# Kernel optimization log

Hardware: AMD Instinct MI355X
Metric: run time of the kernel (lower is better)

## Reference

```python
import jax, jax.numpy as jnp
import numpy as np

B, S, DM = 2, 1024, 2048          # batch, seq_len, hidden_size
H, HKV, D = 16, 8, 128            # heads, kv heads, head_dim
G = H // HKV                      # kv groups
W = 256                           # bmojo window_size
EPS = 1e-6
SCALE = D ** -0.5                 # softmax_scale (set because qk_norm is used)
NEG = -1e30


def _rmsnorm(x, g):
    # per-head RMSNorm over last dim D
    return x * jax.lax.rsqrt(jnp.mean(x * x, axis=-1, keepdims=True) + EPS) * g


def _rope(x, cos, sin):
    # x: [B,S,H,D]; cos/sin: [B,S,D]
    c = cos[:, :, None, :]
    s = sin[:, :, None, :]
    d2 = x.shape[-1] // 2
    x1, x2 = x[..., :d2], x[..., d2:]
    rot = jnp.concatenate([-x2, x1], axis=-1)
    return x * c + rot * s


def setup_inputs() -> dict:
    key = jax.random.key(0)
    ks = jax.random.split(key, 24)
    std = DM ** -0.5

    def lin_w(k, out_d, in_d):
        return jax.random.normal(k, (out_d, in_d), jnp.float32) * std

    def lin_b(k, out_d):
        return jax.random.normal(k, (out_d,), jnp.float32) * 0.01

    inp = {"hidden_states": jax.random.normal(ks[0], (B, S, DM), jnp.float32)}

    # standard RoPE cos/sin tables (theta=10000), shape [B,S,D]
    pos = jnp.arange(S, dtype=jnp.float32)[:, None]
    inv = 1.0 / (10000.0 ** (jnp.arange(0, D, 2, dtype=jnp.float32) / D))
    emb = jnp.concatenate([pos * inv[None, :]] * 2, axis=-1)  # [S,D]
    inp["cos"] = jnp.broadcast_to(jnp.cos(emb)[None], (B, S, D))
    inp["sin"] = jnp.broadcast_to(jnp.sin(emb)[None], (B, S, D))

    # tied (in-context) projections; attention_bias default -> qkv bias True, o bias False
    inp["Wq"] = lin_w(ks[1], H * D, DM);    inp["bq"] = lin_b(ks[2], H * D)
    inp["Wk"] = lin_w(ks[3], HKV * D, DM);  inp["bk"] = lin_b(ks[4], HKV * D)
    inp["Wv"] = lin_w(ks[5], HKV * D, DM);  inp["bv"] = lin_b(ks[6], HKV * D)
    # untied (fading) projections (tie_attn_weights=False)
    inp["Wq2"] = lin_w(ks[7], H * D, DM);   inp["bq2"] = lin_b(ks[8], H * D)
    inp["Wk2"] = lin_w(ks[9], HKV * D, DM); inp["bk2"] = lin_b(ks[10], HKV * D)
    inp["Wv2"] = lin_w(ks[11], HKV * D, DM); inp["bv2"] = lin_b(ks[12], HKV * D)
    inp["Wo"] = lin_w(ks[13], DM, H * D)
    # QK RMSNorm gammas (near-one so grads are nontrivial)
    inp["gq"] = 1.0 + 0.02 * jax.random.normal(ks[14], (D,), jnp.float32)
    inp["gk"] = 1.0 + 0.02 * jax.random.normal(ks[15], (D,), jnp.float32)
    inp["gq2"] = 1.0 + 0.02 * jax.random.normal(ks[16], (D,), jnp.float32)
    inp["gk2"] = 1.0 + 0.02 * jax.random.normal(ks[17], (D,), jnp.float32)
    return inp


def _qkv(x, cos, sin, Wq, bq, Wk, bk, Wv, bv, gq, gk):
    b, s, _ = x.shape
    q = (x @ Wq.T + bq).reshape(b, s, H, D)
    k = (x @ Wk.T + bk).reshape(b, s, HKV, D)
    v = (x @ Wv.T + bv).reshape(b, s, HKV, D)
    q = _rmsnorm(q, gq)
    k = _rmsnorm(k, gk)
    q = _rope(q, cos, sin)
    k = _rope(k, cos, sin)
    # GQA: expand kv heads to H
    k = jnp.repeat(k, G, axis=2)
    v = jnp.repeat(v, G, axis=2)
    return q, k, v


def reference(hidden_states, cos, sin, Wq, bq, Wk, bk, Wv, bv,
              Wq2, bq2, Wk2, bk2, Wv2, bv2, Wo, gq, gk, gq2, gk2):
    # in-context (tied) and fading (untied) projection paths
    q_ic, k_ic, v_ic = _qkv(hidden_states, cos, sin, Wq, bq, Wk, bk, Wv, bv, gq, gk)
    q_f, k_f, v_f = _qkv(hidden_states, cos, sin, Wq2, bq2, Wk2, bk2, Wv2, bv2, gq2, gk2)

    s_ic = jnp.einsum('bqhd,bkhd->bhqk', q_ic, k_ic) * SCALE
    s_f = jnp.einsum('bqhd,bkhd->bhqk', q_f, k_f) * SCALE

    i = jnp.arange(S)[:, None]
    j = jnp.arange(S)[None, :]
    dij = i - j
    in_window = (dij >= 0) & (dij < W)   # sliding window (window_size-1 lookback + self)
    fading = dij >= W                    # older tokens handled by fading memory

    s_ic = jnp.where(in_window, s_ic, NEG)
    s_f = jnp.where(fading, s_f, NEG)

    # joint softmax over the union of window and fading key sets
    p = jax.nn.softmax(jnp.concatenate([s_ic, s_f], axis=-1), axis=-1)  # [B,H,S,2S]
    p_ic, p_f = p[..., :S], p[..., S:]

    out = jnp.einsum('bhqk,bkhd->bqhd', p_ic, v_ic) \
        + jnp.einsum('bhqk,bkhd->bqhd', p_f, v_f)
    out = out.reshape(B, S, H * D)
    return out @ Wo.T
```

## Files before the change

### kernel.cpp

```cpp
#include <hip/hip_runtime.h>
#include <cstdint>
#include <cstddef>

#define B_    2
#define S_    1024
#define DM_   2048
#define H_    16
#define HKV_  8
#define D_    128
#define W_    256
#define NPROJ 8192
#define MROWS 2048
#define SCALE_ 0.08838834764831845f
#define MNEG  -3.0e38f
#define FIXM  16.0f

typedef float  f32x4  __attribute__((ext_vector_type(4)));
typedef __bf16 bf16x8 __attribute__((ext_vector_type(8)));
typedef __bf16 bf16x4 __attribute__((ext_vector_type(4)));

__device__ __forceinline__ void gload16(const void* g, void* l) {
  __builtin_amdgcn_global_load_lds((const __attribute__((address_space(1))) unsigned int*)g,
                                   (__attribute__((address_space(3))) unsigned int*)l, 16, 0, 0);
}

__global__ __launch_bounds__(256) void cvt_all(
    const float* __restrict__ x,  const float* __restrict__ wq,  const float* __restrict__ wk,
    const float* __restrict__ wv, const float* __restrict__ wq2, const float* __restrict__ wk2,
    const float* __restrict__ wv2,const float* __restrict__ wo,
    const float* __restrict__ bq, const float* __restrict__ bk, const float* __restrict__ bv,
    const float* __restrict__ bq2,const float* __restrict__ bk2,const float* __restrict__ bv2,
    __bf16* __restrict__ xb, __bf16* __restrict__ wall, __bf16* __restrict__ wob,
    float* __restrict__ biasA) {
  const int i = blockIdx.x * 256 + threadIdx.x;
  if (i >= 6293504) return;
  if (i >= 6291456) {
    const int j = i - 6291456, flat = j * 4;
    const int set = flat >> 12, off = flat & 4095;
    const float* bsrc; int boff;
    if (off < 2048)      { bsrc = set ? bq2 : bq; boff = off; }
    else if (off < 3072) { bsrc = set ? bk2 : bk; boff = off - 2048; }
    else                 { bsrc = set ? bv2 : bv; boff = off - 3072; }
    ((f32x4*)biasA)[j] = *(const f32x4*)&bsrc[boff];
    return;
  }
  const float* s; __bf16* d;
  if      (i < 1048576) { s = x   + (size_t)i * 4;              d = xb   + (size_t)i * 4; }
  else if (i < 2097152) { s = wq  + (size_t)(i - 1048576) * 4;  d = wall + (size_t)(i - 1048576) * 4; }
  else if (i < 2621440) { s = wk  + (size_t)(i - 2097152) * 4;  d = wall + 4194304  + (size_t)(i - 2097152) * 4; }
  else if (i < 3145728) { s = wv  + (size_t)(i - 2621440) * 4;  d = wall + 6291456  + (size_t)(i - 2621440) * 4; }
  else if (i < 4194304) { s = wq2 + (size_t)(i - 3145728) * 4;  d = wall + 8388608  + (size_t)(i - 3145728) * 4; }
  else if (i < 4718592) { s = wk2 + (size_t)(i - 4194304) * 4;  d = wall + 12582912 + (size_t)(i - 4194304) * 4; }
  else if (i < 5242880) { s = wv2 + (size_t)(i - 4718592) * 4;  d = wall + 14680064 + (size_t)(i - 4718592) * 4; }
  else                  { s = wo  + (size_t)(i - 5242880) * 4;  d = wob  + (size_t)(i - 5242880) * 4; }
  float4 f = *(const float4*)s;
  bf16x4 o;
  o.x = (__bf16)f.x; o.y = (__bf16)f.y; o.z = (__bf16)f.z; o.w = (__bf16)f.w;
  *(bf16x4*)d = o;
}

__global__ __launch_bounds__(512) void gemm_qkv(const __bf16* __restrict__ A,
                                                const __bf16* __restrict__ Bm,
                                                __bf16* __restrict__ Cv,
                                                const float* __restrict__ bias,
                                                int N, int K, int nxp) {
  __shared__ __align__(16) char lds[131072];
  const int tid = threadIdx.x, lane = tid & 63, wid = tid >> 6;
  const int bid = blockIdx.x, xcd = bid & 7, ii = bid >> 3;
  const int x = xcd * nxp + (ii % nxp);
  const int y = ii / nxp;
  const int m0 = y * 256, n0 = x * 256;
  const int wm = (wid >> 2) * 128, wn = (wid & 3) * 64;
  const int g = lane >> 4, c16 = lane & 15;

  int sRow[8], sCol[8]; bool sA[8];
#pragma unroll
  for (int p = 0; p < 8; ++p) {
    const int o = p * 8192 + tid * 16, ro = o & 32767;
    sA[p]   = o < 32768;
    sRow[p] = ro >> 7;
    sCol[p] = (((ro & 127) ^ ((sRow[p] & 7) << 4))) >> 1;
  }

  auto stage2 = [&](int k0, int buf, int q) {
#pragma unroll
    for (int pp = 0; pp < 2; ++pp) {
      const int p = q * 2 + pp;
      const __bf16* src = sA[p] ? &A [(size_t)(m0 + sRow[p]) * K + k0 + sCol[p]]
                                : &Bm[(size_t)(n0 + sRow[p]) * K + k0 + sCol[p]];
      gload16(src, lds + buf * 65536 + p * 8192 + wid * 1024);
    }
  };
  auto rdA = [&](int buf, int mi, int kk) -> bf16x8 {
    const int r = wm + mi * 16 + c16;
    return *(const bf16x8*)(lds + buf * 65536 + r * 128 + ((kk * 64 + g * 16) ^ ((r & 7) << 4)));
  };
  auto rdB = [&](int buf, int ni, int kk) -> bf16x8 {
    const int r = wn + ni * 16 + c16;
    return *(const bf16x8*)(lds + buf * 65536 + 32768 + r * 128 + ((kk * 64 + g * 16) ^ ((r & 7) << 4)));
  };

  f32x4 acc[8][4] = {};
  const int NT = K >> 6;

#pragma unroll
  for (int q = 0; q < 4; ++q) stage2(0, 0, q);
  asm volatile("s_waitcnt vmcnt(0)" ::: "memory");
  __builtin_amdgcn_s_barrier();

  for (int t = 0; t < NT; ++t) {
    const int buf = t & 1, k0 = t * 64;
    bf16x8 b[4][2];
#pragma unroll
    for (int q = 0; q < 4; ++q) {
      bf16x8 a[2][2];
#pragma unroll
      for (int dm = 0; dm < 2; ++dm)
#pragma unroll
        for (int kk = 0; kk < 2; ++kk) a[dm][kk] = rdA(buf, q * 2 + dm, kk);
      if (q == 0) {
#pragma unroll
        for (int ni = 0; ni < 4; ++ni)
#pragma unroll
          for (int kk = 0; kk < 2; ++kk) b[ni][kk] = rdB(buf, ni, kk);
      }
      if (t + 1 < NT) stage2(k0 + 64, buf ^ 1, q);
      __builtin_amdgcn_s_barrier();
      __builtin_amdgcn_s_setprio(1);
#pragma unroll
      for (int dm = 0; dm < 2; ++dm)
#pragma unroll
        for (int ni = 0; ni < 4; ++ni)
#pragma unroll
          for (int kk = 0; kk < 2; ++kk)
            acc[q * 2 + dm][ni] =
              __builtin_amdgcn_mfma_f32_16x16x32_bf16(a[dm][kk], b[ni][kk], acc[q * 2 + dm][ni], 0, 0, 0);
      __builtin_amdgcn_s_setprio(0);
    }
    if (t + 1 < NT) { asm volatile("s_waitcnt vmcnt(0)" ::: "memory"); }
    __builtin_amdgcn_s_barrier();
  }

#pragma unroll
  for (int mi = 0; mi < 8; ++mi)
#pragma unroll
    for (int ni = 0; ni < 4; ++ni) {
      const int gn = n0 + wn + ni * 16 + c16;
      const float bv = bias[gn];
#pragma unroll
      for (int r = 0; r < 4; ++r) {
        const int gm = m0 + wm + mi * 16 + g * 4 + r;
        Cv[(size_t)gm * N + gn] = (__bf16)(acc[mi][ni][r] + bv);
      }
    }
}

__global__ __launch_bounds__(256) void gemm_out(const __bf16* __restrict__ A,
                                                const __bf16* __restrict__ Bm,
                                                float* __restrict__ Cv) {
  __shared__ __align__(16) char lds[65536];
  const int tid = threadIdx.x, lane = tid & 63, wid = tid >> 6;
  const int bid = blockIdx.x, xcd = bid & 7, ii = bid >> 3;
  const int x = xcd * 2 + (ii & 1);
  const int y = ii >> 1;
  const int m0 = y * 128, n0 = x * 128;
  const int wm = (wid >> 1) * 64, wn = (wid & 1) * 64;
  const int g = lane >> 4, c16 = lane & 15;
  const int K = DM_, N = DM_;

  const int tR = tid >> 3;
  const int tC = (((tid & 7) * 16) ^ ((tR & 7) << 4)) >> 1;

  auto stageP = [&](int k0, int buf, int p) {
    const __bf16* src = (p < 4) ? &A [(size_t)(m0 + p * 32 + tR) * K + k0 + tC]
                                : &Bm[(size_t)(n0 + (p - 4) * 32 + tR) * K + k0 + tC];
    gload16(src, lds + buf * 32768 + p * 4096 + wid * 1024);
  };
  auto rdA = [&](int buf, int mi, int kk) -> bf16x8 {
    const int r = wm + mi * 16 + c16;
    return *(const bf16x8*)(lds + buf * 32768 + r * 128 + ((kk * 64 + g * 16) ^ ((r & 7) << 4)));
  };
  auto rdB = [&](int buf, int ni, int kk) -> bf16x8 {
    const int r = wn + ni * 16 + c16;
    return *(const bf16x8*)(lds + buf * 32768 + 16384 + r * 128 + ((kk * 64 + g * 16) ^ ((r & 7) << 4)));
  };

  f32x4 acc[4][4] = {};
  const int NT = K >> 6;

#pragma unroll
  for (int p = 0; p < 8; ++p) stageP(0, 0, p);
  asm volatile("s_waitcnt vmcnt(0)" ::: "memory");
  __builtin_amdgcn_s_barrier();

  for (int t = 0; t < NT; ++t) {
    const int buf = t & 1, k0 = t * 64;
    bf16x8 b[4][2];
#pragma unroll
    for (int q = 0; q < 4; ++q) {
      bf16x8 a[2];
#pragma unroll
      for (int kk = 0; kk < 2; ++kk) a[kk] = rdA(buf, q, kk);
      if (q == 0) {
#pragma unroll
        for (int ni = 0; ni < 4; ++ni)
#pragma unroll
          for (int kk = 0; kk < 2; ++kk) b[ni][kk] = rdB(buf, ni, kk);
      }
      if (t + 1 < NT) { stageP(k0 + 64, buf ^ 1, q * 2); stageP(k0 + 64, buf ^ 1, q * 2 + 1); }
      __builtin_amdgcn_s_barrier();
      __builtin_amdgcn_s_setprio(1);
#pragma unroll
      for (int ni = 0; ni < 4; ++ni)
#pragma unroll
        for (int kk = 0; kk < 2; ++kk)
          acc[q][ni] = __builtin_amdgcn_mfma_f32_16x16x32_bf16(a[kk], b[ni][kk], acc[q][ni], 0, 0, 0);
      __builtin_amdgcn_s_setprio(0);
    }
    if (t + 1 < NT) { asm volatile("s_waitcnt vmcnt(0)" ::: "memory"); }
    __builtin_amdgcn_s_barrier();
  }

#pragma unroll
  for (int mi = 0; mi < 4; ++mi)
#pragma unroll
    for (int ni = 0; ni < 4; ++ni) {
      const int gn = n0 + wn + ni * 16 + c16;
#pragma unroll
      for (int r = 0; r < 4; ++r) {
        const int gm = m0 + wm + mi * 16 + g * 4 + r;
        Cv[(size_t)gm * N + gn] = acc[mi][ni][r];
      }
    }
}

__global__ __launch_bounds__(256) void post_all(const __bf16* __restrict__ proj,
    const float* __restrict__ cosg, const float* __restrict__ sing,
    const float* __restrict__ gq, const float* __restrict__ gk,
    const float* __restrict__ gq2, const float* __restrict__ gk2,
    __bf16* __restrict__ Q0, __bf16* __restrict__ K0,
    __bf16* __restrict__ Q1, __bf16* __restrict__ K1,
    __bf16* __restrict__ Vt0, __bf16* __restrict__ Vt1) {
  __shared__ __bf16 T[64][136];
  const int tid = threadIdx.x;
  if (blockIdx.x < 2048) {
    const int row  = blockIdx.x;
    const int b    = row >> 10;
    const int s    = row & 1023;
    const int lane = tid & 63, wid = tid >> 6;
    const float* cp = cosg + (size_t)row * D_;
    const float* sp = sing + (size_t)row * D_;
    const float c1 = cp[lane], c2 = cp[lane + 64];
    const float s1 = sp[lane], s2 = sp[lane + 64];

    for (int hi = wid; hi < 48; hi += 4) {
      const int  set  = hi >= 24 ? 1 : 0;
      const int  loc  = hi - set * 24;
      const bool isq  = loc < 16;
      const int  head = isq ? loc : loc - 16;
      const __bf16* src = proj + (size_t)row * NPROJ + set * 4096 + (isq ? head * 128 : 2048 + head * 128);
      const float* gv   = set ? (isq ? gq2 : gk2) : (isq ? gq : gk);
      __bf16* dst       = set ? (isq ? Q1 : K1) : (isq ? Q0 : K0);
      const int nheads  = isq ? H_ : HKV_;
      const size_t didx = (((size_t)b * nheads + head) * S_ + s) * D_;
      float x1 = (float)src[lane], x2 = (float)src[lane + 64];
      float ss = x1 * x1 + x2 * x2;
#pragma unroll
      for (int o = 1; o < 64; o <<= 1) ss += __shfl_xor(ss, o);
      const float rr = rsqrtf(ss * (1.f / 128.f) + 1e-6f);
      const float n1 = x1 * rr * gv[lane];
      const float n2 = x2 * rr * gv[lane + 64];
      dst[didx + lane]      = (__bf16)(n1 * c1 - n2 * s1);
      dst[didx + lane + 64] = (__bf16)(n2 * c2 + n1 * s2);
    }
  } else {
    const int bid = blockIdx.x - 2048;
    const int st = bid & 15;
    const int hk = (bid >> 4) & 7;
    const int b  = (bid >> 7) & 1;
    const int sg = bid >> 8;
    const int s0 = st * 64;
    const size_t prow = ((size_t)(b * S_ + s0)) * NPROJ + sg * 4096 + 3072 + hk * 128;
    const int r = tid >> 4, c = (tid & 15) * 8;
#pragma unroll
    for (int pass = 0; pass < 4; ++pass) {
      const int rr = pass * 16 + r;
      *(bf16x8*)&T[rr][c] = *(const bf16x8*)&proj[prow + (size_t)rr * NPROJ + c];
    }
    __syncthreads();
    __bf16* Vt = (sg ? Vt1 : Vt0) + (size_t)(b * HKV_ + hk) * D_ * S_;
    const int d = tid >> 1, half = tid & 1;
#pragma unroll
    for (int q8 = 0; q8 < 4; ++q8) {
      const int sb = half * 32 + q8 * 8;
      bf16x8 v;
#pragma unroll
      for (int k = 0; k < 8; ++k) v[k] = T[sb + k][d];
      *(bf16x8*)&Vt[(size_t)d * S_ + s0 + sb] = v;
    }
  }
}

__global__ __launch_bounds__(256) void attn_fused(
    const __bf16* __restrict__ Q0, const __bf16* __restrict__ K0g, const __bf16* __restrict__ Vt0,
    const __bf16* __restrict__ Q1, const __bf16* __restrict__ K1g, const __bf16* __restrict__ Vt1,
    __bf16* __restrict__ AO) {
  __shared__ __bf16 KsL[2][2][32 * 128];
  __shared__ __bf16 VtL[2][2][128 * 32];
  __shared__ __bf16 Ps[4][16][40];

  const int tid = threadIdx.x, lane = tid & 63, wid = tid >> 6;
  const int bid = blockIdx.x;
  const int xcd = bid & 7, jj = bid >> 3;
  const int combo = xcd * 2 + (jj >> 4);
  const int b = combo >> 3, hk = combo & 7;
  const int h = hk * 2 + ((jj >> 3) & 1);
  const int pq = jj & 7;
  const int qtA = pq, qtB = 15 - pq;
  const int ntA = 2 * qtA + 2;
  const int ntT = 34;

  const int g = lane >> 4, kc = lane & 15;
  const size_t qoff  = (size_t)(b * H_ + h) * S_ * D_;
  const size_t koff  = (size_t)(b * HKV_ + hk) * S_ * D_;
  const size_t vtoff = (size_t)(b * HKV_ + hk) * D_ * S_;

  int kRow[2], kCol[2], vD[2], vJ[2];
#pragma unroll
  for (int p = 0; p < 2; ++p) {
    const int boff = (wid * 2 + p) * 1024 + lane * 16;
    kRow[p] = boff >> 8;
    kCol[p] = ((boff & 255) ^ ((kRow[p] & 7) << 4)) >> 1;
    vD[p]   = boff >> 6;
    vJ[p]   = (boff & 63) >> 1;
  }

  bf16x8 qf0[4], qf1[4];
  auto loadQ = [&](int qw) {
    const int qrow = qw + kc;
#pragma unroll
    for (int c = 0; c < 4; ++c) {
      qf0[c] = *(const bf16x8*)&Q0[qoff + (size_t)qrow * D_ + c * 32 + g * 8];
      qf1[c] = *(const bf16x8*)&Q1[qoff + (size_t)qrow * D_ + c * 32 + g * 8];
    }
  };

  float rs[4];
  f32x4 o[8];
  auto resetS = [&]() {
#pragma unroll
    for (int r = 0; r < 4; ++r) rs[r] = 0.f;
#pragma unroll
    for (int ch = 0; ch < 8; ++ch)
#pragma unroll
      for (int r = 0; r < 4; ++r) o[ch][r] = 0.f;
  };

  auto stage = [&](int qb2, int t, int bufi) {
    const int j0 = t * 32;
    const bool nic = (j0 >= qb2 - 286);
    const bool nf  = (j0 <= qb2 - 193);
#pragma unroll
    for (int p = 0; p < 2; ++p) {
      const int ko = wid * 2048 + p * 1024;
      if (nic) {
        gload16(K0g + koff + (size_t)(j0 + kRow[p]) * D_ + kCol[p], (char*)&KsL[bufi][0][0] + ko);
        gload16(Vt0 + vtoff + (size_t)vD[p] * S_ + j0 + vJ[p],      (char*)&VtL[bufi][0][0] + ko);
      }
      if (nf) {
        gload16(K1g + koff + (size_t)(j0 + kRow[p]) * D_ + kCol[p], (char*)&KsL[bufi][1][0] + ko);
        gload16(Vt1 + vtoff + (size_t)vD[p] * S_ + j0 + vJ[p],      (char*)&VtL[bufi][1][0] + ko);
      }
    }
  };

  auto qk = [&](const __bf16* Kb, const bf16x8 qf[4], f32x4 sv[2]) {
#pragma unroll
    for (int c = 0; c < 4; ++c) {
      const int r0 = kc, r1 = kc + 16;
      const bf16x8 k0f = *(const bf16x8*)((const char*)Kb + r0 * 256 + ((c * 64 + g * 16) ^ ((r0 & 7) << 4)));
      const bf16x8 k1f = *(const bf16x8*)((const char*)Kb + r1 * 256 + ((c * 64 + g * 16) ^ ((r1 & 7) << 4)));
      sv[0] = __builtin_amdgcn_mfma_f32_16x16x32_bf16(qf[c], k0f, sv[0], 0, 0, 0);
      sv[1] = __builtin_amdgcn_mfma_f32_16x16x32_bf16(qf[c], k1f, sv[1], 0, 0, 0);
    }
  };

  auto dopv = [&](const f32x4 sv[2], const __bf16* Vtb) {
#pragma unroll
    for (int nh = 0; nh < 2; ++nh) {
      const int col = kc + nh * 16, c8 = col >> 3, cw = col & 7;
#pragma unroll
      for (int r = 0; r < 4; ++r)
        Ps[wid][g * 4 + r][((c8 ^ g) << 3) + cw] = (__bf16)sv[nh][r];
    }
    asm volatile("s_waitcnt lgkmcnt(0)" ::: "memory");
    const bf16x8 pa = *(const bf16x8*)&Ps[wid][kc][(g ^ (kc >> 2)) << 3];
#pragma unroll
    for (int ch = 0; ch < 8; ++ch) {
      const bf16x8 vb = *(const bf16x8*)&Vtb[(ch * 16 + kc) * 32 + g * 8];
      o[ch] = __builtin_amdgcn_mfma_f32_16x16x32_bf16(pa, vb, o[ch], 0, 0, 0);
    }
  };

  auto writeOut = [&](int qw2) {
    float ell[4];
#pragma unroll
    for (int r = 0; r < 4; ++r) ell[r] = rs[r];
#pragma unroll
    for (int ofs = 1; ofs < 16; ofs <<= 1)
#pragma unroll
      for (int r = 0; r < 4; ++r) ell[r] += __shfl_xor(ell[r], ofs);
#pragma unroll
    for (int r = 0; r < 4; ++r) {
      const float inv = 1.f / ell[r];
      const size_t orow = ((size_t)b * S_ + qw2 + g * 4 + r) * (size_t)(H_ * D_) + h * D_;
#pragma unroll
      for (int ch = 0; ch < 8; ++ch)
        AO[orow + ch * 16 + kc] = (__bf16)(o[ch][r] * inv);
    }
  };

  int qb = qtA * 64, qw = qb + wid * 16;
  loadQ(qw);
  resetS();
  stage(qb, 0, 0);
  asm volatile("s_waitcnt vmcnt(0)" ::: "memory");
  __builtin_amdgcn_s_barrier();
  int cur = 0;

  for (int it = 0; it < ntT; ++it) {
    const int t = (it >= ntA) ? it - ntA : it;
    if (it + 1 < ntT) {
      const bool hN = (it + 1 >= ntA);
      stage(hN ? qtB * 64 : qtA * 64, hN ? it + 1 - ntA : it + 1, cur ^ 1);
    }
    const int j0 = t * 32;
    if (j0 <= qw + 15) {
      const bool w_ic = (j0 >= qw - 286);
      const bool w_f  = (j0 <= qw - 241);

      f32x4 sic[2] = {}, sfd[2] = {};
      if (w_ic) {
        qk(&KsL[cur][0][0], qf0, sic);
#pragma unroll
        for (int nh = 0; nh < 2; ++nh)
#pragma unroll
          for (int r = 0; r < 4; ++r) {
            const int dij = (qw + g * 4 + r) - (j0 + kc + nh * 16);
            const float arg = (dij >= 0 && dij < W_) ? fmaf(sic[nh][r], SCALE_, -FIXM) : MNEG;
            const float p = __expf(arg);
            rs[r] += p; sic[nh][r] = p;
          }
        dopv(sic, &VtL[cur][0][0]);
      }
      if (w_f) {
        qk(&KsL[cur][1][0], qf1, sfd);
#pragma unroll
        for (int nh = 0; nh < 2; ++nh)
#pragma unroll
          for (int r = 0; r < 4; ++r) {
            const int dij = (qw + g * 4 + r) - (j0 + kc + nh * 16);
            const float arg = (dij >= W_) ? fmaf(sfd[nh][r], SCALE_, -FIXM) : MNEG;
            const float p = __expf(arg);
            rs[r] += p; sfd[nh][r] = p;
          }
        dopv(sfd, &VtL[cur][1][0]);
      }
    }
    asm volatile("s_waitcnt vmcnt(0)" ::: "memory");
    __builtin_amdgcn_s_barrier();
    cur ^= 1;

    if (it + 1 == ntA) {
      writeOut(qw);
      resetS();
      qb = qtB * 64; qw = qb + wid * 16;
      loadQ(qw);
    }
  }
  writeOut(qw);
}

extern "C" void kernel_launch(void* const* d_in, const int* in_sizes, int n_in,
                              void* d_out, int out_size, void* d_ws, size_t ws_size,
                              hipStream_t stream) {
  (void)in_sizes; (void)n_in; (void)out_size; (void)ws_size;
  const float* hidden = (const float*)d_in[0];
  const float* cosg   = (const float*)d_in[1];
  const float* sing   = (const float*)d_in[2];
  const float* Wq  = (const float*)d_in[3];
  const float* bq  = (const float*)d_in[4];
  const float* Wk  = (const float*)d_in[5];
  const float* bk  = (const float*)d_in[6];
  const float* Wv  = (const float*)d_in[7];
  const float* bv  = (const float*)d_in[8];
  const float* Wq2 = (const float*)d_in[9];
  const float* bq2 = (const float*)d_in[10];
  const float* Wk2 = (const float*)d_in[11];
  const float* bk2 = (const float*)d_in[12];
  const float* Wv2 = (const float*)d_in[13];
  const float* bv2 = (const float*)d_in[14];
  const float* Wo  = (const float*)d_in[15];
  const float* gq  = (const float*)d_in[16];
  const float* gk  = (const float*)d_in[17];
  const float* gq2 = (const float*)d_in[18];
  const float* gk2 = (const float*)d_in[19];

  char* w = (char*)d_ws;
  __bf16* Xb    = (__bf16*)(w);
  __bf16* Wall  = (__bf16*)(w + 8388608);
  __bf16* Wob   = (__bf16*)(w + 41943040);
  float*  biasA = (float*) (w + 50331648);
  __bf16* proj  = (__bf16*)(w + 50364416);
  __bf16* AO  = Xb;
  __bf16* Q0  = Wall;
  __bf16* Q1  = Wall + 4194304;
  __bf16* K0  = Wall + 8388608;
  __bf16* K1  = Wall + 10485760;
  __bf16* Vt0 = Wall + 12582912;
  __bf16* Vt1 = Wall + 14680064;

  cvt_all<<<24584, 256, 0, stream>>>(hidden, Wq, Wk, Wv, Wq2, Wk2, Wv2, Wo,
                                     bq, bk, bv, bq2, bk2, bv2,
                                     Xb, Wall, Wob, biasA);
  gemm_qkv<<<256, 512, 0, stream>>>(Xb, Wall, proj, biasA, NPROJ, DM_, 4);
  post_all<<<2560, 256, 0, stream>>>(proj, cosg, sing, gq, gk, gq2, gk2,
                                     Q0, K0, Q1, K1, Vt0, Vt1);
  attn_fused<<<256, 256, 0, stream>>>(Q0, K0, Vt0, Q1, K1, Vt1, AO);
  gemm_out<<<256, 256, 0, stream>>>(AO, Wob, (float*)d_out);
}
```

Measured before the change: 177.5 us.

## Restructure GEMM mainloops into 4-stage, 32-wide K pipeline with two-ahead prefetch

Both the QKV projection GEMM and the output GEMM move from a double-buffered 64-wide K step to four LDS stages of 32-wide K slices, prefetching two steps ahead. Each wait now allows some loads to stay in flight (vmcnt(4)) instead of draining all of them. The LDS swizzle changes to a rotation-based layout suited to 64-byte rows. The goal is to hide global-load latency better and avoid full drains every iteration. In exchange there are twice as many barriers per unit of K, and the waitcnt bookkeeping is more fragile.

```diff
diff --git a/kernel.cpp b/kernel.cpp
--- a/kernel.cpp
+++ b/kernel.cpp
@@ -73,72 +73,79 @@
   const int wm = (wid >> 2) * 128, wn = (wid & 3) * 64;
   const int g = lane >> 4, c16 = lane & 15;
 
-  int sRow[8], sCol[8]; bool sA[8];
-#pragma unroll
-  for (int p = 0; p < 8; ++p) {
-    const int o = p * 8192 + tid * 16, ro = o & 32767;
-    sA[p]   = o < 32768;
-    sRow[p] = ro >> 7;
-    sCol[p] = (((ro & 127) ^ ((sRow[p] & 7) << 4))) >> 1;
-  }
-
-  auto stage2 = [&](int k0, int buf, int q) {
-#pragma unroll
-    for (int pp = 0; pp < 2; ++pp) {
-      const int p = q * 2 + pp;
-      const __bf16* src = sA[p] ? &A [(size_t)(m0 + sRow[p]) * K + k0 + sCol[p]]
-                                : &Bm[(size_t)(n0 + sRow[p]) * K + k0 + sCol[p]];
-      gload16(src, lds + buf * 65536 + p * 8192 + wid * 1024);
-    }
-  };
-  auto rdA = [&](int buf, int mi, int kk) -> bf16x8 {
+  int sRow[4], sColE[4]; bool sA4[4];
+#pragma unroll
+  for (int st = 0; st < 4; ++st) {
+    const int o = st * 8192 + tid * 16;
+    sA4[st]  = o < 16384;
+    sRow[st] = (o & 16383) >> 6;
+    const int q = (o >> 4) & 3;
+    sColE[st] = ((q - (sRow[st] >> 1)) & 3) << 3;
+  }
+
+  auto stageStep = [&](int j, int st) {
+    const int s = j & 3;
+    const __bf16* src = sA4[st] ? &A [(size_t)(m0 + sRow[st]) * K + j * 32 + sColE[st]]
+                                : &Bm[(size_t)(n0 + sRow[st]) * K + j * 32 + sColE[st]];
+    gload16(src, lds + s * 32768 + st * 8192 + wid * 1024);
+  };
+  auto rdA = [&](int s, int mi) -> bf16x8 {
     const int r = wm + mi * 16 + c16;
-    return *(const bf16x8*)(lds + buf * 65536 + r * 128 + ((kk * 64 + g * 16) ^ ((r & 7) << 4)));
-  };
-  auto rdB = [&](int buf, int ni, int kk) -> bf16x8 {
+    const int q = (g + (r >> 1)) & 3;
+    return *(const bf16x8*)(lds + s * 32768 + r * 64 + q * 16);
+  };
+  auto rdB = [&](int s, int ni) -> bf16x8 {
     const int r = wn + ni * 16 + c16;
-    return *(const bf16x8*)(lds + buf * 65536 + 32768 + r * 128 + ((kk * 64 + g * 16) ^ ((r & 7) << 4)));
+    const int q = (g + (r >> 1)) & 3;
+    return *(const bf16x8*)(lds + s * 32768 + 16384 + r * 64 + q * 16);
   };
 
   f32x4 acc[8][4] = {};
-  const int NT = K >> 6;
-
-#pragma unroll
-  for (int q = 0; q < 4; ++q) stage2(0, 0, q);
-  asm volatile("s_waitcnt vmcnt(0)" ::: "memory");
+  const int NS = K >> 5;
+
+#pragma unroll
+  for (int st = 0; st < 4; ++st) stageStep(0, st);
+#pragma unroll
+  for (int st = 0; st < 4; ++st) stageStep(1, st);
+  asm volatile("s_waitcnt vmcnt(4)" ::: "memory");
   __builtin_amdgcn_s_barrier();
 
-  for (int t = 0; t < NT; ++t) {
-    const int buf = t & 1, k0 = t * 64;
-    bf16x8 b[4][2];
-#pragma unroll
-    for (int q = 0; q < 4; ++q) {
-      bf16x8 a[2][2];
-#pragma unroll
-      for (int dm = 0; dm < 2; ++dm)
-#pragma unroll
-        for (int kk = 0; kk < 2; ++kk) a[dm][kk] = rdA(buf, q * 2 + dm, kk);
-      if (q == 0) {
-#pragma unroll
-        for (int ni = 0; ni < 4; ++ni)
-#pragma unroll
-          for (int kk = 0; kk < 2; ++kk) b[ni][kk] = rdB(buf, ni, kk);
-      }
-      if (t + 1 < NT) stage2(k0 + 64, buf ^ 1, q);
+  for (int j = 0; j < NS; ++j) {
+    const int s = j & 3;
+    const bool more = (j + 2 < NS);
+    bf16x8 bfr[4], a[4];
+
+#pragma unroll
+    for (int mi = 0; mi < 4; ++mi) a[mi] = rdA(s, mi);
+#pragma unroll
+    for (int ni = 0; ni < 4; ++ni) bfr[ni] = rdB(s, ni);
+    if (more) { stageStep(j + 2, 0); stageStep(j + 2, 1); }
+    __builtin_amdgcn_s_barrier();
+    __builtin_amdgcn_s_setprio(1);
+#pragma unroll
+    for (int mi = 0; mi < 4; ++mi)
+#pragma unroll
+      for (int ni = 0; ni < 4; ++ni)
+        acc[mi][ni] = __builtin_amdgcn_mfma_f32_16x16x32_bf16(a[mi], bfr[ni], acc[mi][ni], 0, 0, 0);
+    __builtin_amdgcn_s_setprio(0);
+
+#pragma unroll
+    for (int mi = 0; mi < 4; ++mi) a[mi] = rdA(s, 4 + mi);
+    if (more) { stageStep(j + 2, 2); stageStep(j + 2, 3); }
+    __builtin_amdgcn_s_barrier();
+    __builtin_amdgcn_s_setprio(1);
+#pragma unroll
+    for (int mi = 0; mi < 4; ++mi)
+#pragma unroll
+      for (int ni = 0; ni < 4; ++ni)
+        acc[4 + mi][ni] = __builtin_amdgcn_mfma_f32_16x16x32_bf16(a[mi], bfr[ni], acc[4 + mi][ni], 0, 0, 0);
+    __builtin_amdgcn_s_setprio(0);
+
+    if (j + 1 < NS) {
+      if (more) { asm volatile("s_waitcnt vmcnt(4)" ::: "memory"); }
+      else      { asm volatile("s_waitcnt vmcnt(0)" ::: "memory"); }
       __builtin_amdgcn_s_barrier();
-      __builtin_amdgcn_s_setprio(1);
-#pragma unroll
-      for (int dm = 0; dm < 2; ++dm)
-#pragma unroll
-        for (int ni = 0; ni < 4; ++ni)
-#pragma unroll
-          for (int kk = 0; kk < 2; ++kk)
-            acc[q * 2 + dm][ni] =
-              __builtin_amdgcn_mfma_f32_16x16x32_bf16(a[dm][kk], b[ni][kk], acc[q * 2 + dm][ni], 0, 0, 0);
-      __builtin_amdgcn_s_setprio(0);
-    }
-    if (t + 1 < NT) { asm volatile("s_waitcnt vmcnt(0)" ::: "memory"); }
-    __builtin_amdgcn_s_barrier();
+    }
   }
 
 #pragma unroll
@@ -168,57 +175,79 @@
   const int g = lane >> 4, c16 = lane & 15;
   const int K = DM_, N = DM_;
 
-  const int tR = tid >> 3;
-  const int tC = (((tid & 7) * 16) ^ ((tR & 7) << 4)) >> 1;
-
-  auto stageP = [&](int k0, int buf, int p) {
-    const __bf16* src = (p < 4) ? &A [(size_t)(m0 + p * 32 + tR) * K + k0 + tC]
-                                : &Bm[(size_t)(n0 + (p - 4) * 32 + tR) * K + k0 + tC];
-    gload16(src, lds + buf * 32768 + p * 4096 + wid * 1024);
-  };
-  auto rdA = [&](int buf, int mi, int kk) -> bf16x8 {
+  int sRow[4], sColE[4]; bool sA4[4];
+#pragma unroll
+  for (int st = 0; st < 4; ++st) {
+    const int o = st * 4096 + tid * 16;
+    sA4[st]  = o < 8192;
+    sRow[st] = (o & 8191) >> 6;
+    const int q = (o >> 4) & 3;
+    sColE[st] = ((q - (sRow[st] >> 1)) & 3) << 3;
+  }
+
+  auto stageStep = [&](int j, int st) {
+    const int s = j & 3;
+    const __bf16* src = sA4[st] ? &A [(size_t)(m0 + sRow[st]) * K + j * 32 + sColE[st]]
+                                : &Bm[(size_t)(n0 + sRow[st]) * K + j * 32 + sColE[st]];
+    gload16(src, lds + s * 16384 + st * 4096 + wid * 1024);
+  };
+  auto rdA = [&](int s, int mi) -> bf16x8 {
     const int r = wm + mi * 16 + c16;
-    return *(const bf16x8*)(lds + buf * 32768 + r * 128 + ((kk * 64 + g * 16) ^ ((r & 7) << 4)));
-  };
-  auto rdB = [&](int buf, int ni, int kk) -> bf16x8 {
+    const int q = (g + (r >> 1)) & 3;
+    return *(const bf16x8*)(lds + s * 16384 + r * 64 + q * 16);
+  };
+  auto rdB = [&](int s, int ni) -> bf16x8 {
     const int r = wn + ni * 16 + c16;
-    return *(const bf16x8*)(lds + buf * 32768 + 16384 + r * 128 + ((kk * 64 + g * 16) ^ ((r & 7) << 4)));
+    const int q = (g + (r >> 1)) & 3;
+    return *(const bf16x8*)(lds + s * 16384 + 8192 + r * 64 + q * 16);
   };
 
   f32x4 acc[4][4] = {};
-  const int NT = K >> 6;
-
-#pragma unroll
-  for (int p = 0; p < 8; ++p) stageP(0, 0, p);
-  asm volatile("s_waitcnt vmcnt(0)" ::: "memory");
+  const int NS = K >> 5;
+
+#pragma unroll
+  for (int st = 0; st < 4; ++st) stageStep(0, st);
+#pragma unroll
+  for (int st = 0; st < 4; ++st) stageStep(1, st);
+  asm volatile("s_waitcnt vmcnt(4)" ::: "memory");
   __builtin_amdgcn_s_barrier();
 
-  for (int t = 0; t < NT; ++t) {
-    const int buf = t & 1, k0 = t * 64;
-    bf16x8 b[4][2];
-#pragma unroll
-    for (int q = 0; q < 4; ++q) {
-      bf16x8 a[2];
-#pragma unroll
-      for (int kk = 0; kk < 2; ++kk) a[kk] = rdA(buf, q, kk);
-      if (q == 0) {
-#pragma unroll
-        for (int ni = 0; ni < 4; ++ni)
-#pragma unroll
-          for (int kk = 0; kk < 2; ++kk) b[ni][kk] = rdB(buf, ni, kk);
-      }
-      if (t + 1 < NT) { stageP(k0 + 64, buf ^ 1, q * 2); stageP(k0 + 64, buf ^ 1, q * 2 + 1); }
+  for (int j = 0; j < NS; ++j) {
+    const int s = j & 3;
+    const bool more = (j + 2 < NS);
+    bf16x8 bfr[4], a[2];
+
+#pragma unroll
+    for (int mi = 0; mi < 2; ++mi) a[mi] = rdA(s, mi);
+#pragma unroll
+    for (int ni = 0; ni < 4; ++ni) bfr[ni] = rdB(s, ni);
+    if (more) { stageStep(j + 2, 0); stageStep(j + 2, 1); }
+    __builtin_amdgcn_s_barrier();
+    __builtin_amdgcn_s_setprio(1);
+#pragma unroll
+    for (int mi = 0; mi < 2; ++mi)
+#pragma unroll
+      for (int ni = 0; ni < 4; ++ni)
+        acc[mi][ni] = __builtin_amdgcn_mfma_f32_16x16x32_bf16(a[mi], bfr[ni], acc[mi][ni], 0, 0, 0);
+    __builtin_amdgcn_s_setprio(0);
+
+#pragma unroll
+    for (int mi = 0; mi < 2; ++mi) a[mi] = rdA(s, 2 + mi);
+    if (more) { stageStep(j + 2, 2); stageStep(j + 2, 3); }
+    __builtin_amdgcn_s_barrier();
+    __builtin_amdgcn_s_setprio(1);
+#pragma unroll
+    for (int mi = 0; mi < 2; ++mi)
+#pragma unroll
+      for (int ni = 0; ni < 4; ++ni)
+        acc[2 + mi][ni] = __builtin_amdgcn_mfma_f32_16x16x32_bf16(a[mi], bfr[ni], acc[2 + mi][ni], 0, 0, 0);
+    __builtin_amdgcn_s_setprio(0);
+
+    if (j + 1 < NS) {
+      if (more) { asm volatile("s_waitcnt vmcnt(4)" ::: "memory"); }
+      else      { asm volatile("s_waitcnt vmcnt(0)" ::: "memory"); }
       __builtin_amdgcn_s_barrier();
-      __builtin_amdgcn_s_setprio(1);
-#pragma unroll
-      for (int ni = 0; ni < 4; ++ni)
-#pragma unroll
-        for (int kk = 0; kk < 2; ++kk)
-          acc[q][ni] = __builtin_amdgcn_mfma_f32_16x16x32_bf16(a[kk], b[ni][kk], acc[q][ni], 0, 0, 0);
-      __builtin_amdgcn_s_setprio(0);
-    }
-    if (t + 1 < NT) { asm volatile("s_waitcnt vmcnt(0)" ::: "memory"); }
-    __builtin_amdgcn_s_barrier();
+    }
   }
 
 #pragma unroll
```

Measured after the change: 179.2 us. No clear change (+1.0%).

## Switch QKV GEMM to triple-buffered 32-wide K stages with new LDS swizzle

Applied to the files above, without the earlier changes.

The QKV projection GEMM drops its double-buffered 64-wide K tiles and uses a three-stage ring of 32-wide K tiles. Loads run two stages ahead and are throttled with partial vmcnt waits, so each step needs one barrier instead of five. The LDS layout moves to 64-byte rows with a rotation-based swizzle to avoid bank conflicts, and LDS use drops from 128KB to 96KB. The cost is twice as many loop iterations with less MFMA work per barrier, and the new swizzle may conflict differently.

```diff
diff --git a/kernel.cpp b/kernel.cpp
--- a/kernel.cpp
+++ b/kernel.cpp
@@ -64,7 +64,7 @@
                                                 __bf16* __restrict__ Cv,
                                                 const float* __restrict__ bias,
                                                 int N, int K, int nxp) {
-  __shared__ __align__(16) char lds[131072];
+  __shared__ __align__(16) char lds[98304];
   const int tid = threadIdx.x, lane = tid & 63, wid = tid >> 6;
   const int bid = blockIdx.x, xcd = bid & 7, ii = bid >> 3;
   const int x = xcd * nxp + (ii % nxp);
@@ -73,72 +73,67 @@
   const int wm = (wid >> 2) * 128, wn = (wid & 3) * 64;
   const int g = lane >> 4, c16 = lane & 15;
 
-  int sRow[8], sCol[8]; bool sA[8];
-#pragma unroll
-  for (int p = 0; p < 8; ++p) {
-    const int o = p * 8192 + tid * 16, ro = o & 32767;
-    sA[p]   = o < 32768;
-    sRow[p] = ro >> 7;
-    sCol[p] = (((ro & 127) ^ ((sRow[p] & 7) << 4))) >> 1;
-  }
-
-  auto stage2 = [&](int k0, int buf, int q) {
-#pragma unroll
-    for (int pp = 0; pp < 2; ++pp) {
-      const int p = q * 2 + pp;
-      const __bf16* src = sA[p] ? &A [(size_t)(m0 + sRow[p]) * K + k0 + sCol[p]]
-                                : &Bm[(size_t)(n0 + sRow[p]) * K + k0 + sCol[p]];
-      gload16(src, lds + buf * 65536 + p * 8192 + wid * 1024);
-    }
-  };
-  auto rdA = [&](int buf, int mi, int kk) -> bf16x8 {
+  int sRow[4], sColE[4]; bool sA4[4];
+#pragma unroll
+  for (int st = 0; st < 4; ++st) {
+    const int o = st * 8192 + tid * 16;
+    sA4[st]  = o < 16384;
+    sRow[st] = (o & 16383) >> 6;
+    const int q = (o >> 4) & 3;
+    sColE[st] = ((q - (sRow[st] >> 1)) & 3) << 3;
+  }
+
+  auto stageTile = [&](int j) {
+    const int s = j % 3;
+#pragma unroll
+    for (int st = 0; st < 4; ++st) {
+      const __bf16* src = sA4[st] ? &A [(size_t)(m0 + sRow[st]) * K + j * 32 + sColE[st]]
+                                  : &Bm[(size_t)(n0 + sRow[st]) * K + j * 32 + sColE[st]];
+      gload16(src, lds + s * 32768 + st * 8192 + wid * 1024);
+    }
+  };
+  auto rdA = [&](int s, int mi) -> bf16x8 {
     const int r = wm + mi * 16 + c16;
-    return *(const bf16x8*)(lds + buf * 65536 + r * 128 + ((kk * 64 + g * 16) ^ ((r & 7) << 4)));
-  };
-  auto rdB = [&](int buf, int ni, int kk) -> bf16x8 {
+    const int q = (g + (r >> 1)) & 3;
+    return *(const bf16x8*)(lds + s * 32768 + r * 64 + q * 16);
+  };
+  auto rdB = [&](int s, int ni) -> bf16x8 {
     const int r = wn + ni * 16 + c16;
-    return *(const bf16x8*)(lds + buf * 65536 + 32768 + r * 128 + ((kk * 64 + g * 16) ^ ((r & 7) << 4)));
+    const int q = (g + (r >> 1)) & 3;
+    return *(const bf16x8*)(lds + s * 32768 + 16384 + r * 64 + q * 16);
   };
 
   f32x4 acc[8][4] = {};
-  const int NT = K >> 6;
-
-#pragma unroll
-  for (int q = 0; q < 4; ++q) stage2(0, 0, q);
-  asm volatile("s_waitcnt vmcnt(0)" ::: "memory");
+  const int NS = K >> 5;
+
+  stageTile(0);
+  stageTile(1);
+  asm volatile("s_waitcnt vmcnt(4)" ::: "memory");
   __builtin_amdgcn_s_barrier();
 
-  for (int t = 0; t < NT; ++t) {
-    const int buf = t & 1, k0 = t * 64;
-    bf16x8 b[4][2];
-#pragma unroll
-    for (int q = 0; q < 4; ++q) {
-      bf16x8 a[2][2];
-#pragma unroll
-      for (int dm = 0; dm < 2; ++dm)
-#pragma unroll
-        for (int kk = 0; kk < 2; ++kk) a[dm][kk] = rdA(buf, q * 2 + dm, kk);
-      if (q == 0) {
-#pragma unroll
-        for (int ni = 0; ni < 4; ++ni)
-#pragma unroll
-          for (int kk = 0; kk < 2; ++kk) b[ni][kk] = rdB(buf, ni, kk);
-      }
-      if (t + 1 < NT) stage2(k0 + 64, buf ^ 1, q);
+  for (int j = 0; j < NS; ++j) {
+    const int s = j % 3;
+    if (j + 2 < NS) stageTile(j + 2);
+
+    bf16x8 a[8], bfr[4];
+#pragma unroll
+    for (int mi = 0; mi < 8; ++mi) a[mi] = rdA(s, mi);
+#pragma unroll
+    for (int ni = 0; ni < 4; ++ni) bfr[ni] = rdB(s, ni);
+
+    __builtin_amdgcn_s_setprio(1);
+#pragma unroll
+    for (int mi = 0; mi < 8; ++mi)
+#pragma unroll
+      for (int ni = 0; ni < 4; ++ni)
+        acc[mi][ni] = __builtin_amdgcn_mfma_f32_16x16x32_bf16(a[mi], bfr[ni], acc[mi][ni], 0, 0, 0);
+    __builtin_amdgcn_s_setprio(0);
+
+    if (j + 1 < NS) {
+      if (j + 2 < NS) { asm volatile("s_waitcnt vmcnt(4)" ::: "memory"); }
+      else            { asm volatile("s_waitcnt vmcnt(0)" ::: "memory"); }
       __builtin_amdgcn_s_barrier();
-      __builtin_amdgcn_s_setprio(1);
-#pragma unroll
-      for (int dm = 0; dm < 2; ++dm)
-#pragma unroll
-        for (int ni = 0; ni < 4; ++ni)
-#pragma unroll
-          for (int kk = 0; kk < 2; ++kk)
-            acc[q * 2 + dm][ni] =
-              __builtin_amdgcn_mfma_f32_16x16x32_bf16(a[dm][kk], b[ni][kk], acc[q * 2 + dm][ni], 0, 0, 0);
-      __builtin_amdgcn_s_setprio(0);
-    }
-    if (t + 1 < NT) { asm volatile("s_waitcnt vmcnt(0)" ::: "memory"); }
-    __builtin_amdgcn_s_barrier();
+    }
   }
 
 #pragma unroll
```

After: 183.4 us. 1.03x slower.

## Split attention into one q-tile per block and widen output GEMM to 8 waves

Applied to the files above, without the earlier changes.

The attention kernel no longer pairs two q-tiles (qt and 15-qt) per block for load balance. It now launches 512 blocks, one q-tile each, ordered from the heaviest tile first. The output GEMM moves from 4 to 8 waves per block, with each wave computing a 64x32 sub-tile and staging split into two halves. The aim is more parallelism and latency hiding, at the cost of the explicit load balancing and with smaller per-wave reuse in the GEMM.

```diff
diff --git a/kernel.cpp b/kernel.cpp
--- a/kernel.cpp
+++ b/kernel.cpp
@@ -155,7 +155,7 @@
     }
 }
 
-__global__ __launch_bounds__(256) void gemm_out(const __bf16* __restrict__ A,
+__global__ __launch_bounds__(512) void gemm_out(const __bf16* __restrict__ A,
                                                 const __bf16* __restrict__ Bm,
                                                 float* __restrict__ Cv) {
   __shared__ __align__(16) char lds[65536];
@@ -164,7 +164,7 @@
   const int x = xcd * 2 + (ii & 1);
   const int y = ii >> 1;
   const int m0 = y * 128, n0 = x * 128;
-  const int wm = (wid >> 1) * 64, wn = (wid & 1) * 64;
+  const int wm = (wid >> 2) * 64, wn = (wid & 3) * 32;
   const int g = lane >> 4, c16 = lane & 15;
   const int K = DM_, N = DM_;
 
@@ -172,9 +172,9 @@
   const int tC = (((tid & 7) * 16) ^ ((tR & 7) << 4)) >> 1;
 
   auto stageP = [&](int k0, int buf, int p) {
-    const __bf16* src = (p < 4) ? &A [(size_t)(m0 + p * 32 + tR) * K + k0 + tC]
-                                : &Bm[(size_t)(n0 + (p - 4) * 32 + tR) * K + k0 + tC];
-    gload16(src, lds + buf * 32768 + p * 4096 + wid * 1024);
+    const __bf16* src = (p < 2) ? &A [(size_t)(m0 + p * 64 + tR) * K + k0 + tC]
+                                : &Bm[(size_t)(n0 + (p - 2) * 64 + tR) * K + k0 + tC];
+    gload16(src, lds + buf * 32768 + p * 8192 + wid * 1024);
   };
   auto rdA = [&](int buf, int mi, int kk) -> bf16x8 {
     const int r = wm + mi * 16 + c16;
@@ -185,46 +185,63 @@
     return *(const bf16x8*)(lds + buf * 32768 + 16384 + r * 128 + ((kk * 64 + g * 16) ^ ((r & 7) << 4)));
   };
 
-  f32x4 acc[4][4] = {};
+  f32x4 acc[4][2] = {};
   const int NT = K >> 6;
 
 #pragma unroll
-  for (int p = 0; p < 8; ++p) stageP(0, 0, p);
+  for (int p = 0; p < 4; ++p) stageP(0, 0, p);
   asm volatile("s_waitcnt vmcnt(0)" ::: "memory");
   __builtin_amdgcn_s_barrier();
 
   for (int t = 0; t < NT; ++t) {
     const int buf = t & 1, k0 = t * 64;
-    bf16x8 b[4][2];
-#pragma unroll
-    for (int q = 0; q < 4; ++q) {
-      bf16x8 a[2];
-#pragma unroll
-      for (int kk = 0; kk < 2; ++kk) a[kk] = rdA(buf, q, kk);
-      if (q == 0) {
-#pragma unroll
-        for (int ni = 0; ni < 4; ++ni)
-#pragma unroll
-          for (int kk = 0; kk < 2; ++kk) b[ni][kk] = rdB(buf, ni, kk);
-      }
-      if (t + 1 < NT) { stageP(k0 + 64, buf ^ 1, q * 2); stageP(k0 + 64, buf ^ 1, q * 2 + 1); }
-      __builtin_amdgcn_s_barrier();
-      __builtin_amdgcn_s_setprio(1);
-#pragma unroll
-      for (int ni = 0; ni < 4; ++ni)
+    const bool more = (t + 1 < NT);
+    bf16x8 b[2][2], a[2][2];
+
+#pragma unroll
+    for (int dm = 0; dm < 2; ++dm)
+#pragma unroll
+      for (int kk = 0; kk < 2; ++kk) a[dm][kk] = rdA(buf, dm, kk);
+#pragma unroll
+    for (int ni = 0; ni < 2; ++ni)
+#pragma unroll
+      for (int kk = 0; kk < 2; ++kk) b[ni][kk] = rdB(buf, ni, kk);
+    if (more) { stageP(k0 + 64, buf ^ 1, 0); stageP(k0 + 64, buf ^ 1, 1); }
+    __builtin_amdgcn_s_barrier();
+    __builtin_amdgcn_s_setprio(1);
+#pragma unroll
+    for (int dm = 0; dm < 2; ++dm)
+#pragma unroll
+      for (int ni = 0; ni < 2; ++ni)
 #pragma unroll
         for (int kk = 0; kk < 2; ++kk)
-          acc[q][ni] = __builtin_amdgcn_mfma_f32_16x16x32_bf16(a[kk], b[ni][kk], acc[q][ni], 0, 0, 0);
-      __builtin_amdgcn_s_setprio(0);
-    }
-    if (t + 1 < NT) { asm volatile("s_waitcnt vmcnt(0)" ::: "memory"); }
+          acc[dm][ni] = __builtin_amdgcn_mfma_f32_16x16x32_bf16(a[dm][kk], b[ni][kk], acc[dm][ni], 0, 0, 0);
+    __builtin_amdgcn_s_setprio(0);
+
+#pragma unroll
+    for (int dm = 0; dm < 2; ++dm)
+#pragma unroll
+      for (int kk = 0; kk < 2; ++kk) a[dm][kk] = rdA(buf, 2 + dm, kk);
+    if (more) { stageP(k0 + 64, buf ^ 1, 2); stageP(k0 + 64, buf ^ 1, 3); }
     __builtin_amdgcn_s_barrier();
+    __builtin_amdgcn_s_setprio(1);
+#pragma unroll
+    for (int dm = 0; dm < 2; ++dm)
+#pragma unroll
+      for (int ni = 0; ni < 2; ++ni)
+#pragma unroll
+        for (int kk = 0; kk < 2; ++kk)
+          acc[2 + dm][ni] = __builtin_amdgcn_mfma_f32_16x16x32_bf16(a[dm][kk], b[ni][kk], acc[2 + dm][ni], 0, 0, 0);
+    __builtin_amdgcn_s_setprio(0);
+
+    if (more) { asm volatile("s_waitcnt vmcnt(0)" ::: "memory"); }
+    __builtin_amdgcn_s_barrier();
   }
 
 #pragma unroll
   for (int mi = 0; mi < 4; ++mi)
 #pragma unroll
-    for (int ni = 0; ni < 4; ++ni) {
+    for (int ni = 0; ni < 2; ++ni) {
       const int gn = n0 + wn + ni * 16 + c16;
 #pragma unroll
       for (int r = 0; r < 4; ++r) {
@@ -311,14 +328,13 @@
 
   const int tid = threadIdx.x, lane = tid & 63, wid = tid >> 6;
   const int bid = blockIdx.x;
-  const int xcd = bid & 7, jj = bid >> 3;
-  const int combo = xcd * 2 + (jj >> 4);
-  const int b = combo >> 3, hk = combo & 7;
-  const int h = hk * 2 + ((jj >> 3) & 1);
-  const int pq = jj & 7;
-  const int qtA = pq, qtB = 15 - pq;
-  const int ntA = 2 * qtA + 2;
-  const int ntT = 34;
+  const int xcd = bid & 7, iidx = bid >> 3;
+  const int bh = xcd * 4 + (iidx & 3);
+  const int qt = 15 - (iidx >> 2);
+  const int b = bh >> 4, h = bh & 15, hk = h >> 1;
+  const int qb = qt * 64;
+  const int qw = qb + wid * 16;
+  const int nt = 2 * qt + 2;
 
   const int g = lane >> 4, kc = lane & 15;
   const size_t qoff  = (size_t)(b * H_ + h) * S_ * D_;
@@ -336,30 +352,22 @@
   }
 
   bf16x8 qf0[4], qf1[4];
-  auto loadQ = [&](int qw) {
+  {
     const int qrow = qw + kc;
 #pragma unroll
     for (int c = 0; c < 4; ++c) {
       qf0[c] = *(const bf16x8*)&Q0[qoff + (size_t)qrow * D_ + c * 32 + g * 8];
       qf1[c] = *(const bf16x8*)&Q1[qoff + (size_t)qrow * D_ + c * 32 + g * 8];
     }
-  };
-
-  float rs[4];
-  f32x4 o[8];
-  auto resetS = [&]() {
-#pragma unroll
-    for (int r = 0; r < 4; ++r) rs[r] = 0.f;
-#pragma unroll
-    for (int ch = 0; ch < 8; ++ch)
-#pragma unroll
-      for (int r = 0; r < 4; ++r) o[ch][r] = 0.f;
-  };
-
-  auto stage = [&](int qb2, int t, int bufi) {
+  }
+
+  float rs[4] = {0.f, 0.f, 0.f, 0.f};
+  f32x4 o[8] = {};
+
+  auto stage = [&](int t, int bufi) {
     const int j0 = t * 32;
-    const bool nic = (j0 >= qb2 - 286);
-    const bool nf  = (j0 <= qb2 - 193);
+    const bool nic = (j0 >= qb - 286);
+    const bool nf  = (j0 <= qb - 193);
 #pragma unroll
     for (int p = 0; p < 2; ++p) {
       const int ko = wid * 2048 + p * 1024;
@@ -402,38 +410,13 @@
     }
   };
 
-  auto writeOut = [&](int qw2) {
-    float ell[4];
-#pragma unroll
-    for (int r = 0; r < 4; ++r) ell[r] = rs[r];
-#pragma unroll
-    for (int ofs = 1; ofs < 16; ofs <<= 1)
-#pragma unroll
-      for (int r = 0; r < 4; ++r) ell[r] += __shfl_xor(ell[r], ofs);
-#pragma unroll
-    for (int r = 0; r < 4; ++r) {
-      const float inv = 1.f / ell[r];
-      const size_t orow = ((size_t)b * S_ + qw2 + g * 4 + r) * (size_t)(H_ * D_) + h * D_;
-#pragma unroll
-      for (int ch = 0; ch < 8; ++ch)
-        AO[orow + ch * 16 + kc] = (__bf16)(o[ch][r] * inv);
-    }
-  };
-
-  int qb = qtA * 64, qw = qb + wid * 16;
-  loadQ(qw);
-  resetS();
-  stage(qb, 0, 0);
+  stage(0, 0);
   asm volatile("s_waitcnt vmcnt(0)" ::: "memory");
   __builtin_amdgcn_s_barrier();
   int cur = 0;
 
-  for (int it = 0; it < ntT; ++it) {
-    const int t = (it >= ntA) ? it - ntA : it;
-    if (it + 1 < ntT) {
-      const bool hN = (it + 1 >= ntA);
-      stage(hN ? qtB * 64 : qtA * 64, hN ? it + 1 - ntA : it + 1, cur ^ 1);
-    }
+  for (int t = 0; t < nt; ++t) {
+    if (t + 1 < nt) stage(t + 1, cur ^ 1);
     const int j0 = t * 32;
     if (j0 <= qw + 15) {
       const bool w_ic = (j0 >= qw - 286);
@@ -470,15 +453,23 @@
     asm volatile("s_waitcnt vmcnt(0)" ::: "memory");
     __builtin_amdgcn_s_barrier();
     cur ^= 1;
-
-    if (it + 1 == ntA) {
-      writeOut(qw);
-      resetS();
-      qb = qtB * 64; qw = qb + wid * 16;
-      loadQ(qw);
-    }
-  }
-  writeOut(qw);
+  }
+
+  float ell[4];
+#pragma unroll
+  for (int r = 0; r < 4; ++r) ell[r] = rs[r];
+#pragma unroll
+  for (int ofs = 1; ofs < 16; ofs <<= 1)
+#pragma unroll
+    for (int r = 0; r < 4; ++r) ell[r] += __shfl_xor(ell[r], ofs);
+#pragma unroll
+  for (int r = 0; r < 4; ++r) {
+    const float inv = 1.f / ell[r];
+    const size_t orow = ((size_t)b * S_ + qw + g * 4 + r) * (size_t)(H_ * D_) + h * D_;
+#pragma unroll
+    for (int ch = 0; ch < 8; ++ch)
+      AO[orow + ch * 16 + kc] = (__bf16)(o[ch][r] * inv);
+  }
 }
 
 extern "C" void kernel_launch(void* const* d_in, const int* in_sizes, int n_in,
@@ -526,6 +517,6 @@
   gemm_qkv<<<256, 512, 0, stream>>>(Xb, Wall, proj, biasA, NPROJ, DM_, 4);
   post_all<<<2560, 256, 0, stream>>>(proj, cosg, sing, gq, gk, gq2, gk2,
                                      Q0, K0, Q1, K1, Vt0, Vt1);
-  attn_fused<<<256, 256, 0, stream>>>(Q0, K0, Vt0, Q1, K1, Vt1, AO);
-  gemm_out<<<256, 256, 0, stream>>>(AO, Wob, (float*)d_out);
-}
+  attn_fused<<<512, 256, 0, stream>>>(Q0, K0, Vt0, Q1, K1, Vt1, AO);
+  gemm_out<<<256, 512, 0, stream>>>(AO, Wob, (float*)d_out);
+}
```

After: 172.6 us. 2.7% less time.
